# Optimization experiments

Hardware: AMD Instinct MI355X
Metric: run time of the kernel (lower is better)

The kernel has to match this reference:

```python
import jax, jax.numpy as jnp
import numpy as np

PRIMES = [250007, 250013, 250027, 250031, 250037, 250043, 250049, 250051]
OFFSETS = np.concatenate([[0], np.cumsum(PRIMES)[:-1]]).astype(np.int64)  # [8]
TOTAL_ROWS = int(np.sum(PRIMES))
D_HEAD = 128          # embedding_dim_per_head
E_DIM = 8 * D_HEAD    # total_embedding_dim = 1024
H_DIM = 2560          # hidden_dim
KSIZE = 4             # causal depthwise conv kernel
EPS = 1e-6


def rmsnorm(x, g):
    # torch.nn.RMSNorm: x / sqrt(mean(x^2) + eps) * weight
    return x * jax.lax.rsqrt(jnp.mean(x * x, axis=-1, keepdims=True) + EPS) * g


def setup_inputs() -> dict:
    key = jax.random.key(0)
    ks = jax.random.split(key, 10)
    B, L = 4, 4096
    return {
        "hidden_states": jax.random.normal(ks[0], (B, L, H_DIM), jnp.float32),
        "engram_hash_indices": jax.random.randint(ks[1], (B, L, 8), 0, 250007, jnp.int64),
        "emb_table": jax.random.normal(ks[2], (TOTAL_ROWS, D_HEAD), jnp.float32) * 0.02,
        "w_v": jax.random.normal(ks[3], (H_DIM, E_DIM), jnp.float32) * 0.02,
        "w_k": jax.random.normal(ks[4], (H_DIM, E_DIM), jnp.float32) * 0.02,
        "g_h": jnp.ones((H_DIM,), jnp.float32),
        "g_k": jnp.ones((H_DIM,), jnp.float32),
        "g_v": jnp.ones((H_DIM,), jnp.float32),
        # paper zero-inits the conv; use small random weights so the conv path is exercised
        "conv_w": jax.random.normal(ks[5], (H_DIM, KSIZE), jnp.float32) * 0.02,
        "conv_b": jax.random.normal(ks[6], (H_DIM,), jnp.float32) * 0.02,
    }


def reference(hidden_states, engram_hash_indices, emb_table, w_v, w_k, g_h, g_k, g_v, conv_w, conv_b):
    B, L, H = hidden_states.shape
    # multi-head hash embedding retrieval
    idx = engram_hash_indices + jnp.asarray(OFFSETS)            # [B,L,8]
    e_t = emb_table[idx].reshape(B, L, E_DIM)                    # gather + concat heads
    # value / key projections (Linear, no bias)
    v_t = jnp.einsum('ble,he->blh', e_t, w_v)                    # [B,L,H]
    k_t = jnp.einsum('ble,he->blh', e_t, w_k)
    # context-aware gating
    h_n = rmsnorm(hidden_states, g_h)
    k_n = rmsnorm(k_t, g_k)
    dot = jnp.sum(h_n * k_n, axis=-1) / jnp.sqrt(jnp.float32(H))  # [B,L]
    stable = jnp.sqrt(jnp.maximum(jnp.abs(dot), 1e-6)) * jnp.sign(dot)
    alpha = jax.nn.sigmoid(stable)                               # [B,L]
    v_tilde = alpha[..., None] * v_t                             # [B,L,H]
    v_n = rmsnorm(v_tilde, g_v)
    # causal depthwise conv1d (left pad K-1) + SiLU
    x_pad = jnp.pad(v_n, ((0, 0), (KSIZE - 1, 0), (0, 0)))       # [B,L+3,H]
    conv = sum(conv_w[:, j] * x_pad[:, j:j + L, :] for j in range(KSIZE)) + conv_b
    y = jax.nn.silu(conv) + v_tilde
    return hidden_states + y
```

## Files before the change

### kernel.cpp

```cpp
#include <hip/hip_runtime.h>
#include <cstddef>
#include <cstdint>

typedef __bf16 bf16;
typedef __bf16 bf16x4 __attribute__((ext_vector_type(4)));
typedef __bf16 bf16x8 __attribute__((ext_vector_type(8)));
typedef float f32x4 __attribute__((ext_vector_type(4)));

#define AS1C(p) ((const __attribute__((address_space(1))) void*)(p))
#define AS3(p)  ((__attribute__((address_space(3))) void*)(p))

#define MROWS 16384
#define HDIM 2560
#define EDIM 1024
#define LSEQ 4096

static __device__ const int kHeadOff[8] = {0, 250007, 500020, 750047,
                                           1000078, 1250115, 1500158, 1750207};

__global__ __launch_bounds__(256) void k_gather(const int* __restrict__ hidx,
                                                const float* __restrict__ emb,
                                                bf16* __restrict__ E) {
  const int t = threadIdx.x;
  const int m = blockIdx.x * 2 + (t >> 7);
  const int tt = t & 127;
  const int head = tt >> 4;
  const int e8 = (tt & 15) * 8;
  const int rid = hidx[m * 8 + head] + kHeadOff[head];
  const float4 v0 = *(const float4*)(emb + (size_t)rid * 128 + e8);
  const float4 v1 = *(const float4*)(emb + (size_t)rid * 128 + e8 + 4);
  bf16x8 o;
  o[0] = (bf16)v0.x; o[1] = (bf16)v0.y; o[2] = (bf16)v0.z; o[3] = (bf16)v0.w;
  o[4] = (bf16)v1.x; o[5] = (bf16)v1.y; o[6] = (bf16)v1.z; o[7] = (bf16)v1.w;
  *(bf16x8*)(E + (size_t)m * EDIM + head * 128 + e8) = o;
}

__global__ __launch_bounds__(256) void k_cvt2(const float* __restrict__ s0,
                                              bf16* __restrict__ d0,
                                              const float* __restrict__ s1,
                                              bf16* __restrict__ d1) {
  int b = blockIdx.x;
  const float* src = s0;
  bf16* dst = d0;
  if (b >= 1280) { b -= 1280; src = s1; dst = d1; }
  const int i = (b * 256 + threadIdx.x) * 8;
  float4 a = *(const float4*)(src + i);
  float4 c = *(const float4*)(src + i + 4);
  bf16x8 o;
  o[0] = (bf16)a.x; o[1] = (bf16)a.y; o[2] = (bf16)a.z; o[3] = (bf16)a.w;
  o[4] = (bf16)c.x; o[5] = (bf16)c.y; o[6] = (bf16)c.z; o[7] = (bf16)c.w;
  *(bf16x8*)(dst + i) = o;
}

__device__ __forceinline__ float red16(float v) {
  v += __shfl_xor(v, 1);
  v += __shfl_xor(v, 2);
  v += __shfl_xor(v, 4);
  v += __shfl_xor(v, 8);
  return v;
}


#define LDSB 24576

__global__ __launch_bounds__(512, 4) void k_gemm(const bf16* __restrict__ A,
                                                 const bf16* __restrict__ Wv,
                                                 const bf16* __restrict__ Wk,
                                                 const float* __restrict__ hidden,
                                                 const float* __restrict__ g_h,
                                                 const float* __restrict__ g_k,
                                                 bf16* __restrict__ Vt,
                                                 float* __restrict__ S) {
  __shared__ __attribute__((aligned(16))) char ldsc[3 * LDSB];
  const int tid = threadIdx.x;
  const int wid = tid >> 6, lane = tid & 63;
  const int wm = wid >> 1, wn = wid & 1;
  const int r16 = lane & 15, khalf = lane >> 4;

  const int w = blockIdx.x;
  const int xcd = w & 7;
  const int r_ = w >> 3;
  const int gx = r_ >> 3;
  const int y = xcd * 8 + (r_ & 7);
  const int m0 = y * 256;
  const bool isV = (gx < 20);
  const int n0 = (isV ? gx : gx - 20) * 128;
  const bf16* Wp = isV ? Wv : Wk;

  const int sw = ((r16 >> 1) & 3) << 4;
  const int c0 = (khalf * 16) ^ sw;
  const int aRd = (wm * 64 + r16) * 64 + c0;
  const int bRd = 16384 + (wn * 64 + r16) * 64 + c0;

  const int srow = tid >> 2;
  const int scol = (((tid & 3) ^ ((tid >> 3) & 3))) * 8;
  const bf16* pA0 = A + (size_t)(m0 + srow) * EDIM + scol;
  const bf16* pA1 = pA0 + (size_t)128 * EDIM;
  const bf16* pB = Wp + (size_t)(n0 + srow) * EDIM + scol;
  const int ldsW = wid * 1024;

  f32x4 acc[4][4] = {};

#define STAGE(BUFO, KT) do {                                                   \
    __builtin_amdgcn_global_load_lds(AS1C(pA0 + (KT) * 32),                    \
        AS3(ldsc + (BUFO) + ldsW), 16, 0, 0);                                  \
    __builtin_amdgcn_global_load_lds(AS1C(pA1 + (KT) * 32),                    \
        AS3(ldsc + (BUFO) + 8192 + ldsW), 16, 0, 0);                           \
    __builtin_amdgcn_global_load_lds(AS1C(pB + (KT) * 32),                     \
        AS3(ldsc + (BUFO) + 16384 + ldsW), 16, 0, 0);                          \
    __builtin_amdgcn_sched_barrier(0);                                         \
  } while (0)

#define PHASE(BUFO, STBUF, KT, ST, VMW) do {                                   \
    if (ST) STAGE(STBUF, (KT) + 2);                                            \
    bf16x8 aF[4], bF[4];                                                       \
    _Pragma("unroll") for (int mi = 0; mi < 4; ++mi)                           \
      aF[mi] = *(const bf16x8*)(ldsc + (BUFO) + aRd + mi * 1024);              \
    _Pragma("unroll") for (int nj = 0; nj < 4; ++nj)                           \
      bF[nj] = *(const bf16x8*)(ldsc + (BUFO) + bRd + nj * 1024);              \
    __builtin_amdgcn_s_setprio(1);                                             \
    _Pragma("unroll") for (int nj = 0; nj < 4; ++nj)                           \
      _Pragma("unroll") for (int mi = 0; mi < 4; ++mi)                         \
        acc[mi][nj] = __builtin_amdgcn_mfma_f32_16x16x32_bf16(                 \
            aF[mi], bF[nj], acc[mi][nj], 0, 0, 0);                             \
    __builtin_amdgcn_s_setprio(0);                                             \
    asm volatile("s_waitcnt " VMW " lgkmcnt(0)" ::: "memory");                 \
    __builtin_amdgcn_s_barrier();                                              \
  } while (0)

  STAGE(0, 0);
  STAGE(LDSB, 1);
  asm volatile("s_waitcnt vmcnt(3)" ::: "memory");
  __builtin_amdgcn_s_barrier();

  for (int p = 0; p < 30; p += 3) {
    PHASE(0,        2 * LDSB, p,     true, "vmcnt(3)");
    PHASE(LDSB,     0,        p + 1, true, "vmcnt(3)");
    PHASE(2 * LDSB, LDSB,     p + 2, true, "vmcnt(3)");
  }
  PHASE(0, 0, 30, false, "vmcnt(0)");
  PHASE(LDSB, 0, 31, false, "");

  float* P = (float*)ldsc;
  if (isV) {
#pragma unroll
    for (int mi = 0; mi < 4; ++mi) {
#pragma unroll
      for (int nj = 0; nj < 4; ++nj) {
        const int col = n0 + wn * 64 + nj * 16 + r16;
#pragma unroll
        for (int r = 0; r < 4; ++r) {
          const int row = m0 + wm * 64 + mi * 16 + khalf * 4 + r;
          Vt[(size_t)row * HDIM + col] = (bf16)acc[mi][nj][r];
        }
      }
#pragma unroll
      for (int r = 0; r < 4; ++r) {
        float p = 0.f;
#pragma unroll
        for (int nj = 0; nj < 4; ++nj) p += acc[mi][nj][r] * acc[mi][nj][r];
        p = red16(p);
        if (r16 == 0) {
          const int rl = wm * 64 + mi * 16 + khalf * 4 + r;
          P[wn * 256 + rl] = p;
        }
      }
    }
    __syncthreads();
    if (tid < 256) {
      const float s = P[tid] + P[256 + tid];
      atomicAdd(&S[(size_t)(m0 + tid) * 4 + 3], s);
    }
  } else {
    float ghk[4];
#pragma unroll
    for (int nj = 0; nj < 4; ++nj) {
      const int col = n0 + wn * 64 + nj * 16 + r16;
      ghk[nj] = g_h[col] * g_k[col];
    }
#pragma unroll
    for (int mi = 0; mi < 4; ++mi) {
#pragma unroll
      for (int r = 0; r < 4; ++r) {
        const int row = m0 + wm * 64 + mi * 16 + khalf * 4 + r;
        float p1 = 0.f, p2 = 0.f, p3 = 0.f;
#pragma unroll
        for (int nj = 0; nj < 4; ++nj) {
          const int col = n0 + wn * 64 + nj * 16 + r16;
          const float k = acc[mi][nj][r];
          const float h = hidden[(size_t)row * HDIM + col];
          p1 += h * h;
          p2 += h * ghk[nj] * k;
          p3 += k * k;
        }
        p1 = red16(p1); p2 = red16(p2); p3 = red16(p3);
        if (r16 == 0) {
          const int rl = wm * 64 + mi * 16 + khalf * 4 + r;
          float* Pr = P + (wn * 256 + rl) * 3;
          Pr[0] = p1; Pr[1] = p2; Pr[2] = p3;
        }
      }
    }
    __syncthreads();
    for (int j = tid; j < 768; j += 512) {
      const int rl = j / 3, c = j % 3;
      const float s = P[j] + P[768 + j];
      atomicAdd(&S[(size_t)(m0 + rl) * 4 + c], s);
    }
  }
#undef STAGE
#undef PHASE
}

__device__ __forceinline__ void row_scal(const float* __restrict__ S, int m,
                                         float& alpha, float& av) {
  const float4 s = *(const float4*)(S + (size_t)m * 4);
  const float inv_h = rsqrtf(s.x * (1.f / HDIM) + 1e-6f);
  const float inv_k = rsqrtf(s.z * (1.f / HDIM) + 1e-6f);
  const float dot = s.y * inv_h * inv_k * 0.019764235f;
  float st = sqrtf(fmaxf(fabsf(dot), 1e-6f));
  st = (dot < 0.f) ? -st : st;
  if (dot == 0.f) st = 0.f;
  alpha = 1.f / (1.f + __expf(-st));
  av = alpha * rsqrtf(alpha * alpha * s.w * (1.f / HDIM) + 1e-6f);
}

__global__ __launch_bounds__(320) void k_fuse(const float* __restrict__ hidden,
                                              const bf16* __restrict__ Vt,
                                              const float* __restrict__ S,
                                              const float* __restrict__ g_v,
                                              const float* __restrict__ conv_w,
                                              const float* __restrict__ conv_b,
                                              float* __restrict__ out) {
  const int mbase = blockIdx.x * 8;
  const int l0 = mbase & (LSEQ - 1);
  const int t = threadIdx.x;
  const int h0 = t * 8;

  float gv[8], cb[8];
  *(float4*)&gv[0] = *(const float4*)(g_v + h0);
  *(float4*)&gv[4] = *(const float4*)(g_v + h0 + 4);
  *(float4*)&cb[0] = *(const float4*)(conv_b + h0);
  *(float4*)&cb[4] = *(const float4*)(conv_b + h0 + 4);
  float4 cw[8];
#pragma unroll
  for (int i = 0; i < 8; ++i)
    cw[i] = *(const float4*)(conv_w + (size_t)(h0 + i) * 4);

  float win[4][8];
#pragma unroll
  for (int jj = 0; jj < 4; ++jj)
#pragma unroll
    for (int i = 0; i < 8; ++i) win[jj][i] = 0.f;

#pragma unroll
  for (int j = 0; j < 11; ++j) {
    const int lj = l0 - 3 + j;
    const int m = mbase - 3 + j;
    float vtl[8];
    if (lj >= 0) {
      float alpha, av;
      row_scal(S, m, alpha, av);
      const bf16x8 v = *(const bf16x8*)(Vt + (size_t)m * HDIM + h0);
#pragma unroll
      for (int i = 0; i < 8; ++i) {
        const float vt = (float)v[i];
        vtl[i] = alpha * vt;
        win[j & 3][i] = av * vt * gv[i];
      }
    } else {
#pragma unroll
      for (int i = 0; i < 8; ++i) { win[j & 3][i] = 0.f; vtl[i] = 0.f; }
    }
    if (j >= 3) {
      const int R = mbase + j - 3;
      const size_t base = (size_t)R * HDIM + h0;
      float hx[8];
      *(float4*)&hx[0] = *(const float4*)(hidden + base);
      *(float4*)&hx[4] = *(const float4*)(hidden + base + 4);
      float o[8];
#pragma unroll
      for (int i = 0; i < 8; ++i) {
        float c = cb[i];
        c += ((const float*)&cw[i])[0] * win[(j - 3) & 3][i];
        c += ((const float*)&cw[i])[1] * win[(j - 2) & 3][i];
        c += ((const float*)&cw[i])[2] * win[(j - 1) & 3][i];
        c += ((const float*)&cw[i])[3] * win[j & 3][i];
        const float y = c / (1.f + __expf(-c));
        o[i] = hx[i] + y + vtl[i];
      }
      *(float4*)(out + base) = *(float4*)&o[0];
      *(float4*)(out + base + 4) = *(float4*)&o[4];
    }
  }
}

extern "C" void kernel_launch(void* const* d_in, const int* in_sizes, int n_in,
                              void* d_out, int out_size, void* d_ws,
                              size_t ws_size, hipStream_t stream) {
  const float* hidden = (const float*)d_in[0];
  const int* hashidx = (const int*)d_in[1];
  const float* emb = (const float*)d_in[2];
  const float* w_v = (const float*)d_in[3];
  const float* w_k = (const float*)d_in[4];
  const float* g_h = (const float*)d_in[5];
  const float* g_k = (const float*)d_in[6];
  const float* g_v = (const float*)d_in[7];
  const float* conv_w = (const float*)d_in[8];
  const float* conv_b = (const float*)d_in[9];
  float* out = (float*)d_out;

  char* w = (char*)d_ws;
  bf16* e16 = (bf16*)w;  w += (size_t)MROWS * EDIM * 2;
  bf16* wv16 = (bf16*)w; w += (size_t)HDIM * EDIM * 2;
  bf16* wk16 = (bf16*)w; w += (size_t)HDIM * EDIM * 2;
  bf16* vt16 = (bf16*)w; w += (size_t)MROWS * HDIM * 2;
  float* S = (float*)w;  w += (size_t)MROWS * 4 * 4;

  hipMemsetAsync(S, 0, (size_t)MROWS * 4 * 4, stream);
  k_gather<<<MROWS / 2, 256, 0, stream>>>(hashidx, emb, e16);
  k_cvt2<<<2560, 256, 0, stream>>>(w_v, wv16, w_k, wk16);
  k_gemm<<<dim3(2560), 512, 0, stream>>>(e16, wv16, wk16, hidden, g_h, g_k,
                                         vt16, S);
  k_fuse<<<MROWS / 8, 320, 0, stream>>>(hidden, vt16, S, g_v, conv_w, conv_b,
                                        out);
}
```

Measured before the change: 329.7 us.

## Fuse prep kernels and switch GEMM to 32x32 MFMA with double buffering

Merges the gather, weight conversion and S-zeroing memset into one prep kernel to cut launch overhead. The GEMM moves from 16x16x32 to 32x32x16 bf16 MFMA tiles, which lowers LDS fragment traffic per FLOP. The LDS pipeline goes from triple to double buffering, with barriers placed before each compute phase. Epilogue reductions are reworked for the 32-lane output layout. Double buffering reduces overlap between global loads and compute, but the smaller LDS footprint may allow more blocks per CU.

```diff
diff --git a/kernel.cpp b/kernel.cpp
--- a/kernel.cpp
+++ b/kernel.cpp
@@ -3,9 +3,8 @@
 #include <cstdint>
 
 typedef __bf16 bf16;
-typedef __bf16 bf16x4 __attribute__((ext_vector_type(4)));
 typedef __bf16 bf16x8 __attribute__((ext_vector_type(8)));
-typedef float f32x4 __attribute__((ext_vector_type(4)));
+typedef float f32x16 __attribute__((ext_vector_type(16)));
 
 #define AS1C(p) ((const __attribute__((address_space(1))) void*)(p))
 #define AS3(p)  ((__attribute__((address_space(3))) void*)(p))
@@ -18,45 +17,52 @@
 static __device__ const int kHeadOff[8] = {0, 250007, 500020, 750047,
                                            1000078, 1250115, 1500158, 1750207};
 
-__global__ __launch_bounds__(256) void k_gather(const int* __restrict__ hidx,
-                                                const float* __restrict__ emb,
-                                                bf16* __restrict__ E) {
+__global__ __launch_bounds__(256) void k_prep(const int* __restrict__ hidx,
+                                              const float* __restrict__ emb,
+                                              bf16* __restrict__ E,
+                                              const float* __restrict__ wv,
+                                              bf16* __restrict__ wv16,
+                                              const float* __restrict__ wk,
+                                              bf16* __restrict__ wk16,
+                                              float* __restrict__ S) {
+  const int b = blockIdx.x;
   const int t = threadIdx.x;
-  const int m = blockIdx.x * 2 + (t >> 7);
-  const int tt = t & 127;
-  const int head = tt >> 4;
-  const int e8 = (tt & 15) * 8;
-  const int rid = hidx[m * 8 + head] + kHeadOff[head];
-  const float4 v0 = *(const float4*)(emb + (size_t)rid * 128 + e8);
-  const float4 v1 = *(const float4*)(emb + (size_t)rid * 128 + e8 + 4);
-  bf16x8 o;
-  o[0] = (bf16)v0.x; o[1] = (bf16)v0.y; o[2] = (bf16)v0.z; o[3] = (bf16)v0.w;
-  o[4] = (bf16)v1.x; o[5] = (bf16)v1.y; o[6] = (bf16)v1.z; o[7] = (bf16)v1.w;
-  *(bf16x8*)(E + (size_t)m * EDIM + head * 128 + e8) = o;
-}
-
-__global__ __launch_bounds__(256) void k_cvt2(const float* __restrict__ s0,
-                                              bf16* __restrict__ d0,
-                                              const float* __restrict__ s1,
-                                              bf16* __restrict__ d1) {
-  int b = blockIdx.x;
-  const float* src = s0;
-  bf16* dst = d0;
-  if (b >= 1280) { b -= 1280; src = s1; dst = d1; }
-  const int i = (b * 256 + threadIdx.x) * 8;
-  float4 a = *(const float4*)(src + i);
-  float4 c = *(const float4*)(src + i + 4);
-  bf16x8 o;
-  o[0] = (bf16)a.x; o[1] = (bf16)a.y; o[2] = (bf16)a.z; o[3] = (bf16)a.w;
-  o[4] = (bf16)c.x; o[5] = (bf16)c.y; o[6] = (bf16)c.z; o[7] = (bf16)c.w;
-  *(bf16x8*)(dst + i) = o;
-}
-
-__device__ __forceinline__ float red16(float v) {
+  if (b < 8192) {
+    const int m = b * 2 + (t >> 7);
+    const int tt = t & 127;
+    const int head = tt >> 4;
+    const int e8 = (tt & 15) * 8;
+    const int rid = hidx[m * 8 + head] + kHeadOff[head];
+    const float4 v0 = *(const float4*)(emb + (size_t)rid * 128 + e8);
+    const float4 v1 = *(const float4*)(emb + (size_t)rid * 128 + e8 + 4);
+    bf16x8 o;
+    o[0] = (bf16)v0.x; o[1] = (bf16)v0.y; o[2] = (bf16)v0.z; o[3] = (bf16)v0.w;
+    o[4] = (bf16)v1.x; o[5] = (bf16)v1.y; o[6] = (bf16)v1.z; o[7] = (bf16)v1.w;
+    *(bf16x8*)(E + (size_t)m * EDIM + head * 128 + e8) = o;
+  } else if (b < 10752) {
+    int bb = b - 8192;
+    const float* src = wv;
+    bf16* dst = wv16;
+    if (bb >= 1280) { bb -= 1280; src = wk; dst = wk16; }
+    const int i = (bb * 256 + t) * 8;
+    const float4 a = *(const float4*)(src + i);
+    const float4 c = *(const float4*)(src + i + 4);
+    bf16x8 o;
+    o[0] = (bf16)a.x; o[1] = (bf16)a.y; o[2] = (bf16)a.z; o[3] = (bf16)a.w;
+    o[4] = (bf16)c.x; o[5] = (bf16)c.y; o[6] = (bf16)c.z; o[7] = (bf16)c.w;
+    *(bf16x8*)(dst + i) = o;
+  } else {
+    const int i = ((b - 10752) * 256 + t) * 4;
+    *(float4*)(S + i) = float4{0.f, 0.f, 0.f, 0.f};
+  }
+}
+
+__device__ __forceinline__ float red32(float v) {
   v += __shfl_xor(v, 1);
   v += __shfl_xor(v, 2);
   v += __shfl_xor(v, 4);
   v += __shfl_xor(v, 8);
+  v += __shfl_xor(v, 16);
   return v;
 }
 
@@ -71,11 +77,11 @@
                                                  const float* __restrict__ g_k,
                                                  bf16* __restrict__ Vt,
                                                  float* __restrict__ S) {
-  __shared__ __attribute__((aligned(16))) char ldsc[3 * LDSB];
+  __shared__ __attribute__((aligned(16))) char ldsc[2 * LDSB];
   const int tid = threadIdx.x;
   const int wid = tid >> 6, lane = tid & 63;
   const int wm = wid >> 1, wn = wid & 1;
-  const int r16 = lane & 15, khalf = lane >> 4;
+  const int l31 = lane & 31, hi = lane >> 5;
 
   const int w = blockIdx.x;
   const int xcd = w & 7;
@@ -87,10 +93,10 @@
   const int n0 = (isV ? gx : gx - 20) * 128;
   const bf16* Wp = isV ? Wv : Wk;
 
-  const int sw = ((r16 >> 1) & 3) << 4;
-  const int c0 = (khalf * 16) ^ sw;
-  const int aRd = (wm * 64 + r16) * 64 + c0;
-  const int bRd = 16384 + (wn * 64 + r16) * 64 + c0;
+  const int sw = ((l31 >> 1) & 3) << 4;
+  const int c0s = (hi * 16) ^ sw;
+  const int aRd = (wm * 64 + l31) * 64 + c0s;
+  const int bRd = 16384 + (wn * 64 + l31) * 64 + c0s;
 
   const int srow = tid >> 2;
   const int scol = (((tid & 3) ^ ((tid >> 3) & 3))) * 8;
@@ -99,7 +105,7 @@
   const bf16* pB = Wp + (size_t)(n0 + srow) * EDIM + scol;
   const int ldsW = wid * 1024;
 
-  f32x4 acc[4][4] = {};
+  f32x16 acc[2][2] = {};
 
 #define STAGE(BUFO, KT) do {                                                   \
     __builtin_amdgcn_global_load_lds(AS1C(pA0 + (KT) * 32),                    \
@@ -111,57 +117,77 @@
     __builtin_amdgcn_sched_barrier(0);                                         \
   } while (0)
 
-#define PHASE(BUFO, STBUF, KT, ST, VMW) do {                                   \
-    if (ST) STAGE(STBUF, (KT) + 2);                                            \
-    bf16x8 aF[4], bF[4];                                                       \
-    _Pragma("unroll") for (int mi = 0; mi < 4; ++mi)                           \
-      aF[mi] = *(const bf16x8*)(ldsc + (BUFO) + aRd + mi * 1024);              \
-    _Pragma("unroll") for (int nj = 0; nj < 4; ++nj)                           \
-      bF[nj] = *(const bf16x8*)(ldsc + (BUFO) + bRd + nj * 1024);              \
+#define PHASE_CORE(BUFO) do {                                                  \
+    bf16x8 aF[2][2], bF[2][2];                                                 \
+    _Pragma("unroll") for (int mi = 0; mi < 2; ++mi) {                         \
+      aF[mi][0] = *(const bf16x8*)(ldsc + (BUFO) + aRd + mi * 2048);           \
+      aF[mi][1] = *(const bf16x8*)(ldsc + (BUFO) + (aRd ^ 32) + mi * 2048);    \
+    }                                                                          \
+    _Pragma("unroll") for (int nj = 0; nj < 2; ++nj) {                         \
+      bF[nj][0] = *(const bf16x8*)(ldsc + (BUFO) + bRd + nj * 2048);           \
+      bF[nj][1] = *(const bf16x8*)(ldsc + (BUFO) + (bRd ^ 32) + nj * 2048);    \
+    }                                                                          \
     __builtin_amdgcn_s_setprio(1);                                             \
-    _Pragma("unroll") for (int nj = 0; nj < 4; ++nj)                           \
-      _Pragma("unroll") for (int mi = 0; mi < 4; ++mi)                         \
-        acc[mi][nj] = __builtin_amdgcn_mfma_f32_16x16x32_bf16(                 \
-            aF[mi], bF[nj], acc[mi][nj], 0, 0, 0);                             \
+    _Pragma("unroll") for (int ks = 0; ks < 2; ++ks)                           \
+      _Pragma("unroll") for (int nj = 0; nj < 2; ++nj)                         \
+        _Pragma("unroll") for (int mi = 0; mi < 2; ++mi)                       \
+          acc[mi][nj] = __builtin_amdgcn_mfma_f32_32x32x16_bf16(               \
+              aF[mi][ks], bF[nj][ks], acc[mi][nj], 0, 0, 0);                   \
     __builtin_amdgcn_s_setprio(0);                                             \
-    asm volatile("s_waitcnt " VMW " lgkmcnt(0)" ::: "memory");                 \
+    asm volatile("s_waitcnt lgkmcnt(0)" ::: "memory");                         \
     __builtin_amdgcn_s_barrier();                                              \
   } while (0)
 
+#define BEGIN3() do {                                                          \
+    asm volatile("s_waitcnt vmcnt(3)" ::: "memory");                           \
+    __builtin_amdgcn_s_barrier();                                              \
+    asm volatile("" ::: "memory");                                             \
+  } while (0)
+
+#define BEGIN0() do {                                                          \
+    asm volatile("s_waitcnt vmcnt(0)" ::: "memory");                           \
+    __builtin_amdgcn_s_barrier();                                              \
+    asm volatile("" ::: "memory");                                             \
+  } while (0)
+
   STAGE(0, 0);
   STAGE(LDSB, 1);
-  asm volatile("s_waitcnt vmcnt(3)" ::: "memory");
-  __builtin_amdgcn_s_barrier();
-
-  for (int p = 0; p < 30; p += 3) {
-    PHASE(0,        2 * LDSB, p,     true, "vmcnt(3)");
-    PHASE(LDSB,     0,        p + 1, true, "vmcnt(3)");
-    PHASE(2 * LDSB, LDSB,     p + 2, true, "vmcnt(3)");
+
+  for (int p = 0; p < 30; p += 2) {
+    BEGIN3();
+    PHASE_CORE(0);
+    STAGE(0, p + 2);
+    BEGIN3();
+    PHASE_CORE(LDSB);
+    STAGE(LDSB, p + 3);
   }
-  PHASE(0, 0, 30, false, "vmcnt(0)");
-  PHASE(LDSB, 0, 31, false, "");
+  BEGIN3();
+  PHASE_CORE(0);
+  BEGIN0();
+  PHASE_CORE(LDSB);
 
   float* P = (float*)ldsc;
   if (isV) {
 #pragma unroll
-    for (int mi = 0; mi < 4; ++mi) {
-#pragma unroll
-      for (int nj = 0; nj < 4; ++nj) {
-        const int col = n0 + wn * 64 + nj * 16 + r16;
-#pragma unroll
-        for (int r = 0; r < 4; ++r) {
-          const int row = m0 + wm * 64 + mi * 16 + khalf * 4 + r;
-          Vt[(size_t)row * HDIM + col] = (bf16)acc[mi][nj][r];
+    for (int mi = 0; mi < 2; ++mi) {
+#pragma unroll
+      for (int nj = 0; nj < 2; ++nj) {
+        const int col = n0 + wn * 64 + nj * 32 + l31;
+#pragma unroll
+        for (int reg = 0; reg < 16; ++reg) {
+          const int row =
+              m0 + wm * 64 + mi * 32 + (reg & 3) + 8 * (reg >> 2) + 4 * hi;
+          Vt[(size_t)row * HDIM + col] = (bf16)acc[mi][nj][reg];
         }
       }
 #pragma unroll
-      for (int r = 0; r < 4; ++r) {
-        float p = 0.f;
-#pragma unroll
-        for (int nj = 0; nj < 4; ++nj) p += acc[mi][nj][r] * acc[mi][nj][r];
-        p = red16(p);
-        if (r16 == 0) {
-          const int rl = wm * 64 + mi * 16 + khalf * 4 + r;
+      for (int reg = 0; reg < 16; ++reg) {
+        float p = acc[mi][0][reg] * acc[mi][0][reg] +
+                  acc[mi][1][reg] * acc[mi][1][reg];
+        p = red32(p);
+        if (l31 == 0) {
+          const int rl =
+              wm * 64 + mi * 32 + (reg & 3) + 8 * (reg >> 2) + 4 * hi;
           P[wn * 256 + rl] = p;
         }
       }
@@ -172,30 +198,26 @@
       atomicAdd(&S[(size_t)(m0 + tid) * 4 + 3], s);
     }
   } else {
-    float ghk[4];
-#pragma unroll
-    for (int nj = 0; nj < 4; ++nj) {
-      const int col = n0 + wn * 64 + nj * 16 + r16;
-      ghk[nj] = g_h[col] * g_k[col];
-    }
-#pragma unroll
-    for (int mi = 0; mi < 4; ++mi) {
-#pragma unroll
-      for (int r = 0; r < 4; ++r) {
-        const int row = m0 + wm * 64 + mi * 16 + khalf * 4 + r;
-        float p1 = 0.f, p2 = 0.f, p3 = 0.f;
-#pragma unroll
-        for (int nj = 0; nj < 4; ++nj) {
-          const int col = n0 + wn * 64 + nj * 16 + r16;
-          const float k = acc[mi][nj][r];
-          const float h = hidden[(size_t)row * HDIM + col];
-          p1 += h * h;
-          p2 += h * ghk[nj] * k;
-          p3 += k * k;
-        }
-        p1 = red16(p1); p2 = red16(p2); p3 = red16(p3);
-        if (r16 == 0) {
-          const int rl = wm * 64 + mi * 16 + khalf * 4 + r;
+    const int col0 = n0 + wn * 64 + l31;
+    const int col1 = col0 + 32;
+    const float ghk0 = g_h[col0] * g_k[col0];
+    const float ghk1 = g_h[col1] * g_k[col1];
+#pragma unroll
+    for (int mi = 0; mi < 2; ++mi) {
+#pragma unroll
+      for (int reg = 0; reg < 16; ++reg) {
+        const int row =
+            m0 + wm * 64 + mi * 32 + (reg & 3) + 8 * (reg >> 2) + 4 * hi;
+        const float h0 = hidden[(size_t)row * HDIM + col0];
+        const float h1 = hidden[(size_t)row * HDIM + col1];
+        const float k0 = acc[mi][0][reg], k1 = acc[mi][1][reg];
+        float p1 = h0 * h0 + h1 * h1;
+        float p2 = h0 * ghk0 * k0 + h1 * ghk1 * k1;
+        float p3 = k0 * k0 + k1 * k1;
+        p1 = red32(p1); p2 = red32(p2); p3 = red32(p3);
+        if (l31 == 0) {
+          const int rl =
+              wm * 64 + mi * 32 + (reg & 3) + 8 * (reg >> 2) + 4 * hi;
           float* Pr = P + (wn * 256 + rl) * 3;
           Pr[0] = p1; Pr[1] = p2; Pr[2] = p3;
         }
@@ -209,7 +231,9 @@
     }
   }
 #undef STAGE
-#undef PHASE
+#undef PHASE_CORE
+#undef BEGIN3
+#undef BEGIN0
 }
 
 __device__ __forceinline__ void row_scal(const float* __restrict__ S, int m,
@@ -317,9 +341,7 @@
   bf16* vt16 = (bf16*)w; w += (size_t)MROWS * HDIM * 2;
   float* S = (float*)w;  w += (size_t)MROWS * 4 * 4;
 
-  hipMemsetAsync(S, 0, (size_t)MROWS * 4 * 4, stream);
-  k_gather<<<MROWS / 2, 256, 0, stream>>>(hashidx, emb, e16);
-  k_cvt2<<<2560, 256, 0, stream>>>(w_v, wv16, w_k, wk16);
+  k_prep<<<10816, 256, 0, stream>>>(hashidx, emb, e16, w_v, wv16, w_k, wk16, S);
   k_gemm<<<dim3(2560), 512, 0, stream>>>(e16, wv16, wk16, hidden, g_h, g_k,
                                          vt16, S);
   k_fuse<<<MROWS / 8, 320, 0, stream>>>(hidden, vt16, S, g_v, conv_w, conv_b,
```

New measurement: 377.6 us. 1.15x slower.
